# Performance work log

Hardware: AMD Instinct MI355X
Metric: run time of the kernel (lower is better)

The kernel has to match this reference:

```python
import jax, jax.numpy as jnp
import numpy as np

EPS = 1e-12  # torch F.normalize eps

def _l2norm(x):
    n = jnp.linalg.norm(x, axis=-1, keepdims=True)
    return x / jnp.maximum(n, EPS)

def _encode(h, mask, W, b):
    # h: [B,S,H], mask: [B,S] int
    h = h * mask[..., None].astype(h.dtype)      # zero padded tokens
    pooled = h[:, 0]                             # pooling_type='cls'
    col = h[:, 1:] @ W + b                       # colbert_linear on tokens 1:
    return _l2norm(pooled), _l2norm(col)         # normalize=True


def setup_inputs() -> dict:
    key = jax.random.key(0)
    k1, k2, k3, k4, k5, k6 = jax.random.split(key, 6)
    Q, Sq, C, Sc, H, D = 64, 32, 256, 256, 768, 128
    return {
        "q_hidden": jax.random.normal(k1, (Q, Sq, H), jnp.float32),
        "c_hidden": jax.random.normal(k2, (C, Sc, H), jnp.float32),
        "W": jax.random.normal(k3, (H, D), jnp.float32) / np.sqrt(H).astype(np.float32),
        "b": jax.random.normal(k4, (D,), jnp.float32) * 0.01,
        "q_mask": jax.random.randint(k5, (Q, Sq), 0, 2, jnp.int32),
        "c_mask": jax.random.randint(k6, (C, Sc), 0, 2, jnp.int32),
    }


def reference(q_hidden, c_hidden, W, b, q_mask, c_mask):
    q_pooled, q_col = _encode(q_hidden, q_mask, W, b)   # q_col: [Q, Sq-1, D]
    c_pooled, c_col = _encode(c_hidden, c_mask, W, b)   # c_col: [C, Sc-1, D]
    # MaxSim late interaction (get_batch_colbert_sim)
    token_sim = jnp.einsum('qin,cjn->qicj', q_col, c_col)  # [Q, Sq-1, C, Sc-1]
    sim = token_sim.max(axis=-1)                           # max over doc tokens j
    denom = q_mask[:, 1:].sum(-1, keepdims=True).astype(sim.dtype)
    sim = sim.sum(axis=1) / denom                          # [Q, C]
    return sim, q_pooled, c_pooled
```

## Files before the change

kernel.cpp:

```cpp
#include <hip/hip_runtime.h>
#include <hip/hip_bf16.h>

#define QN 64
#define SQ 32
#define CN 256
#define SC 256
#define HD 768
#define DD 128

typedef __attribute__((ext_vector_type(8))) short short8;
typedef __attribute__((ext_vector_type(4))) float f32x4;

static __device__ __forceinline__ unsigned short f2bf(float x) {
  unsigned u = __float_as_uint(x);
  unsigned r = 0x7FFFu + ((u >> 16) & 1u);
  return (unsigned short)((u + r) >> 16);
}
static __device__ __forceinline__ unsigned pack2(float a, float b) {
  return (unsigned)f2bf(a) | ((unsigned)f2bf(b) << 16);
}

typedef const __attribute__((address_space(1))) unsigned int* as1_u32p;
typedef __attribute__((address_space(3))) unsigned int* as3_u32p;
static __device__ __forceinline__ void gl_lds16(const void* g, void* l) {
  __builtin_amdgcn_global_load_lds((as1_u32p)g, (as3_u32p)l, 16, 0, 0);
}

__global__ __launch_bounds__(256) void prep_kernel(
    const float* __restrict__ W,
    const float* __restrict__ qh, const int* __restrict__ qm,
    const float* __restrict__ ch, const int* __restrict__ cm,
    unsigned short* __restrict__ WtS,
    float* __restrict__ outq, float* __restrict__ outc,
    unsigned short* __restrict__ qcolP) {
  __shared__ float red[4];
  int bid = blockIdx.x, tid = threadIdx.x;

  if (bid < DD) {
    int d = bid;
    if (tid < 96) {
      int kc = tid;
      unsigned p[4];
#pragma unroll
      for (int e = 0; e < 4; ++e) {
        float a = W[(size_t)(kc * 8 + 2 * e) * DD + d];
        float b = W[(size_t)(kc * 8 + 2 * e + 1) * DD + d];
        p[e] = pack2(a, b);
      }
      int kcp = (kc & ~7) | ((kc & 7) ^ (d & 7));
      *(uint4*)&WtS[((size_t)d * 96 + kcp) * 8] = *(uint4*)p;
    }
    return;
  }

  int row = bid - DD;
  const float* src;
  float* dst;
  float m;
  if (row < QN) {
    src = qh + (size_t)row * SQ * HD;
    m = (float)qm[row * SQ];
    dst = outq + (size_t)row * HD;
  } else {
    int b = row - QN;
    src = ch + (size_t)b * SC * HD;
    m = (float)cm[b * SC];
    dst = outc + (size_t)b * HD;
  }
  float ss = 0.f;
  for (int k = tid; k < HD; k += 256) {
    float v = src[k] * m;
    ss += v * v;
  }
  int lane = tid & 63, wv = tid >> 6;
  for (int off = 32; off; off >>= 1) ss += __shfl_xor(ss, off);
  if (lane == 0) red[wv] = ss;
  __syncthreads();
  float tot = red[0] + red[1] + red[2] + red[3];
  float inv = 1.f / fmaxf(sqrtf(tot), 1e-12f);
  for (int k = tid; k < HD; k += 256) dst[k] = src[k] * m * inv;
  if (row < QN && tid < 64)
    ((unsigned*)(qcolP + ((size_t)row * 32 + 31) * DD))[tid] = 0u;
}

union ProjLDS {
  unsigned short b[128 * 32 * 8];
  float cep[128 * 132];
};

__global__ __launch_bounds__(256, 2) void proj_kernel(
    const float* __restrict__ q_hidden, const float* __restrict__ c_hidden,
    const int* __restrict__ q_mask, const int* __restrict__ c_mask,
    const unsigned short* __restrict__ WtS, const float* __restrict__ bias,
    unsigned short* __restrict__ qcol, unsigned short* __restrict__ ccol) {
  __shared__ ProjLDS u;
  int bx = blockIdx.x;
  int isQ = (bx >= 510) ? 1 : 0;
  int base = isQ ? (bx - 510) : bx;
  int tid = threadIdx.x, lane = tid & 63, wv = tid >> 6;
  int lm = lane & 15, lq = lane >> 4;

  const float* hrow[2];
#pragma unroll
  for (int mt = 0; mt < 2; ++mt) {
    int g = base * 128 + wv * 32 + mt * 16 + lm;
    const float* hp;
    if (isQ) {
      g = (g < 1983) ? g : 1983;
      int qq = g / 31, t = g - qq * 31;
      hp = q_hidden + ((size_t)qq * SQ + t + 1) * HD;
    } else {
      int cb = g / 255, t = g - cb * 255;
      hp = c_hidden + ((size_t)cb * SC + t + 1) * HD;
    }
    hrow[mt] = hp;
  }

  f32x4 acc[2][8];
#pragma unroll
  for (int i = 0; i < 2; ++i)
#pragma unroll
    for (int j = 0; j < 8; ++j) acc[i][j] = (f32x4){0.f, 0.f, 0.f, 0.f};

  for (int stage = 0; stage < 3; ++stage) {
    __syncthreads();
#pragma unroll
    for (int i = 0; i < 16; ++i) {
      int d = i * 8 + wv * 2 + (lane >> 5);
      int lc = lane & 31;
      gl_lds16(WtS + ((size_t)d * 96 + stage * 32 + lc) * 8,
               (char*)u.b + (size_t)(i * 256 + wv * 64) * 16);
    }
    __syncthreads();

#pragma unroll
    for (int w = 0; w < 8; ++w) {
      int kwin = stage * 8 + w;
      short8 afr[2];
#pragma unroll
      for (int mt = 0; mt < 2; ++mt) {
        const float* ha = hrow[mt] + kwin * 32 + lq * 8;
        float4 a0 = *(const float4*)ha;
        float4 a1 = *(const float4*)(ha + 4);
        unsigned p[4];
        p[0] = pack2(a0.x, a0.y); p[1] = pack2(a0.z, a0.w);
        p[2] = pack2(a1.x, a1.y); p[3] = pack2(a1.z, a1.w);
        afr[mt] = *(short8*)p;
      }
      int t = w * 4 + lq;
      int lcp = (t & ~7) | ((t & 7) ^ (lm & 7));
      short8 bfr[8];
#pragma unroll
      for (int nt = 0; nt < 8; ++nt) {
        int ci = (nt * 16 + lm) * 32 + lcp;
        bfr[nt] = *(const short8*)&u.b[(size_t)ci * 8];
      }
#pragma unroll
      for (int mt = 0; mt < 2; ++mt)
#pragma unroll
        for (int nt = 0; nt < 8; ++nt)
          acc[mt][nt] = __builtin_amdgcn_mfma_f32_16x16x32_bf16(afr[mt], bfr[nt], acc[mt][nt], 0, 0, 0);
    }
  }

  __syncthreads();
#pragma unroll
  for (int mt = 0; mt < 2; ++mt)
#pragma unroll
    for (int nt = 0; nt < 8; ++nt)
#pragma unroll
      for (int r = 0; r < 4; ++r) {
        int rw = wv * 32 + mt * 16 + lq * 4 + r;
        int col = nt * 16 + lm;
        u.cep[rw * 132 + col] = acc[mt][nt][r];
      }
  __syncthreads();

  int tk = tid >> 1, hf = tid & 1;
  int g = base * 128 + tk;
  int qq, t, valid = 1;
  float fm;
  if (isQ) {
    if (g >= 1983) { valid = (g == 1983); g = 1983; }
    qq = g / 31; t = g - qq * 31;
    fm = (float)q_mask[qq * SQ + t + 1];
  } else {
    qq = g / 255; t = g - qq * 255;
    fm = (float)c_mask[qq * SC + t + 1];
  }

  float v[64];
  float ss = 0.f;
#pragma unroll
  for (int j = 0; j < 16; ++j) {
    float4 cv = *(const float4*)&u.cep[tk * 132 + hf * 64 + j * 4];
    float4 bv = *(const float4*)&bias[hf * 64 + j * 4];
    v[4 * j + 0] = cv.x * fm + bv.x; v[4 * j + 1] = cv.y * fm + bv.y;
    v[4 * j + 2] = cv.z * fm + bv.z; v[4 * j + 3] = cv.w * fm + bv.w;
#pragma unroll
    for (int e = 0; e < 4; ++e) ss += v[4 * j + e] * v[4 * j + e];
  }
  ss += __shfl_xor(ss, 1);
  float inv = 1.f / fmaxf(sqrtf(ss), 1e-12f);

  uint4 pk4[8];
#pragma unroll
  for (int j = 0; j < 8; ++j) {
    unsigned p[4];
#pragma unroll
    for (int e = 0; e < 4; ++e)
      p[e] = pack2(v[8 * j + 2 * e] * inv, v[8 * j + 2 * e + 1] * inv);
    pk4[j] = *(uint4*)p;
  }

  if (isQ) {
    if (valid) {
      uint4* dst = (uint4*)(qcol + ((size_t)qq * 32 + t) * DD + hf * 64);
#pragma unroll
      for (int j = 0; j < 8; ++j) dst[j] = pk4[j];
    }
  } else {
    uint4* rowp = (uint4*)(ccol + ((size_t)qq * 256 + t) * DD);
#pragma unroll
    for (int j = 0; j < 8; ++j) {
      int kc = hf * 8 + j;
      int p = (kc & 8) | ((kc & 7) ^ (t & 7));
      rowp[p] = pk4[j];
    }
    if (t == 254) {
      uint4* rowp2 = rowp + 8;
#pragma unroll
      for (int j = 0; j < 8; ++j) {
        int kc = hf * 8 + j;
        int p = (kc & 8) | ((kc & 7) ^ 7);
        rowp2[p] = pk4[j];
      }
    }
  }
}

__global__ __launch_bounds__(256, 2) void sim_kernel(
    const unsigned short* __restrict__ qcolP,
    const unsigned short* __restrict__ ccol,
    const int* __restrict__ qmask,
    float* __restrict__ sim) {
  __shared__ unsigned short cbuf[256 * 128];
  int tid = threadIdx.x, lane = tid & 63, wv = tid >> 6;
  int lm = lane & 15, lq = lane >> 4;
  int qb = blockIdx.y * 8 + wv * 2;
  int c0 = blockIdx.x * 4;

  short8 af[2][2][4];
#pragma unroll
  for (int q2 = 0; q2 < 2; ++q2)
#pragma unroll
    for (int it = 0; it < 2; ++it)
#pragma unroll
      for (int kf = 0; kf < 4; ++kf)
        af[q2][it][kf] = *(const short8*)(qcolP +
            (((size_t)(qb + q2) * 32 + it * 16 + lm) * DD + kf * 32 + lq * 8));

  float dinv[2];
#pragma unroll
  for (int q2 = 0; q2 < 2; ++q2) {
    float v = (lane >= 1 && lane < 32) ? (float)qmask[(qb + q2) * SQ + lane] : 0.f;
    for (int off = 1; off < 64; off <<= 1) v += __shfl_xor(v, off);
    dinv[q2] = 1.f / v;
  }

  for (int cc = 0; cc < 4; ++cc) {
    int c = c0 + cc;
    __syncthreads();
    const unsigned short* src = ccol + (size_t)c * SC * DD;
#pragma unroll
    for (int i = 0; i < 16; ++i) {
      gl_lds16(src + (size_t)(i * 256 + wv * 64 + lane) * 8,
               (char*)cbuf + (size_t)(i * 256 + wv * 64) * 16);
    }
    __syncthreads();

    float rmax[2][2];
#pragma unroll
    for (int q2 = 0; q2 < 2; ++q2) { rmax[q2][0] = -__builtin_inff(); rmax[q2][1] = -__builtin_inff(); }

    for (int jt = 0; jt < 16; ++jt) {
      short8 cf[4];
#pragma unroll
      for (int kf = 0; kf < 4; ++kf) {
        int row = jt * 16 + lm;
        int kc = kf * 4 + lq;
        int p = (kc & 8) | ((kc & 7) ^ (row & 7));
        cf[kf] = *(const short8*)&cbuf[(size_t)(row * 16 + p) * 8];
      }
#pragma unroll
      for (int q2 = 0; q2 < 2; ++q2)
#pragma unroll
        for (int it = 0; it < 2; ++it) {
          f32x4 acc = (f32x4){0.f, 0.f, 0.f, 0.f};
#pragma unroll
          for (int kf = 0; kf < 4; ++kf)
            acc = __builtin_amdgcn_mfma_f32_16x16x32_bf16(cf[kf], af[q2][it][kf], acc, 0, 0, 0);
          float loc = fmaxf(fmaxf(acc[0], acc[1]), fmaxf(acc[2], acc[3]));
          rmax[q2][it] = fmaxf(rmax[q2][it], loc);
        }
    }

#pragma unroll
    for (int q2 = 0; q2 < 2; ++q2) {
      float m0 = rmax[q2][0], m1 = rmax[q2][1];
      m0 = fmaxf(m0, __shfl_xor(m0, 16)); m0 = fmaxf(m0, __shfl_xor(m0, 32));
      m1 = fmaxf(m1, __shfl_xor(m1, 16)); m1 = fmaxf(m1, __shfl_xor(m1, 32));
      float s = m0 + ((lm == 15) ? 0.f : m1);
      s += __shfl_xor(s, 1); s += __shfl_xor(s, 2);
      s += __shfl_xor(s, 4); s += __shfl_xor(s, 8);
      if (lane == 0) sim[(qb + q2) * CN + c] = s * dinv[q2];
    }
  }
}

extern "C" void kernel_launch(void* const* d_in, const int* in_sizes, int n_in,
                              void* d_out, int out_size, void* d_ws, size_t ws_size,
                              hipStream_t stream) {
  const float* q_hidden = (const float*)d_in[0];
  const float* c_hidden = (const float*)d_in[1];
  const float* W = (const float*)d_in[2];
  const float* bias = (const float*)d_in[3];
  const int* q_mask = (const int*)d_in[4];
  const int* c_mask = (const int*)d_in[5];

  float* out = (float*)d_out;
  float* sim = out;
  float* q_pooled = out + QN * CN;
  float* c_pooled = q_pooled + QN * HD;

  unsigned short* WtS   = (unsigned short*)d_ws;
  unsigned short* qcolP = (unsigned short*)((char*)d_ws + (256 << 10));
  unsigned short* ccol  = (unsigned short*)((char*)d_ws + (1 << 20));

  prep_kernel<<<DD + QN + CN, 256, 0, stream>>>(W, q_hidden, q_mask, c_hidden, c_mask,
                                                WtS, q_pooled, c_pooled, qcolP);
  proj_kernel<<<526, 256, 0, stream>>>(q_hidden, c_hidden, q_mask, c_mask,
                                       WtS, bias, qcolP, ccol);
  sim_kernel<<<dim3(64, 8), 256, 0, stream>>>(qcolP, ccol, q_mask, sim);
}
```

Measured before the change: 374.7 us.

## Stage activations via LDS in projection and enlarge per-wave query tile in sim

The projection kernel now copies fp32 activation tiles and bf16 weight tiles into shared memory with async global-to-LDS loads over 12 k-steps, using swizzled indexing, instead of reading activations straight from global memory per wave. Its epilogue is split into two 64-row halves so the LDS union shrinks, and launch bounds rise to 3 blocks per CU to allow more occupancy. The sim kernel gives each wave 4 queries over 2 docs instead of 2 queries over 4 docs, which reuses each loaded doc tile across more queries. The cost is more barriers per k-loop in the projection kernel and higher register pressure in sim from the larger query fragment array.

Measured after the change: 363.7 us. 1.03x faster.

```diff
diff --git a/kernel.cpp b/kernel.cpp
--- a/kernel.cpp
+++ b/kernel.cpp
@@ -84,11 +84,11 @@
 }
 
 union ProjLDS {
-  unsigned short b[128 * 32 * 8];
-  float cep[128 * 132];
+  struct { float a[128 * 64]; unsigned short w[128 * 64]; } s;
+  float cep[64 * 132];
 };
 
-__global__ __launch_bounds__(256, 2) void proj_kernel(
+__global__ __launch_bounds__(256, 3) void proj_kernel(
     const float* __restrict__ q_hidden, const float* __restrict__ c_hidden,
     const int* __restrict__ q_mask, const int* __restrict__ c_mask,
     const unsigned short* __restrict__ WtS, const float* __restrict__ bias,
@@ -100,10 +100,12 @@
   int tid = threadIdx.x, lane = tid & 63, wv = tid >> 6;
   int lm = lane & 15, lq = lane >> 4;
 
-  const float* hrow[2];
-#pragma unroll
-  for (int mt = 0; mt < 2; ++mt) {
-    int g = base * 128 + wv * 32 + mt * 16 + lm;
+  int ac = (tid & 8) | ((tid & 7) ^ ((tid >> 4) & 7));
+  const float* aptr[8];
+#pragma unroll
+  for (int i = 0; i < 8; ++i) {
+    int r = i * 16 + (tid >> 4);
+    int g = base * 128 + r;
     const float* hp;
     if (isQ) {
       g = (g < 1983) ? g : 1983;
@@ -113,7 +115,13 @@
       int cb = g / 255, t = g - cb * 255;
       hp = c_hidden + ((size_t)cb * SC + t + 1) * HD;
     }
-    hrow[mt] = hp;
+    aptr[i] = hp + ac * 4;
+  }
+  const unsigned short* wptr[4];
+#pragma unroll
+  for (int i = 0; i < 4; ++i) {
+    int d = i * 32 + (tid >> 3);
+    wptr[i] = WtS + ((size_t)d * 96 + (tid & 7)) * 8;
   }
 
   f32x4 acc[2][8];
@@ -122,38 +130,37 @@
 #pragma unroll
     for (int j = 0; j < 8; ++j) acc[i][j] = (f32x4){0.f, 0.f, 0.f, 0.f};
 
-  for (int stage = 0; stage < 3; ++stage) {
-    __syncthreads();
-#pragma unroll
-    for (int i = 0; i < 16; ++i) {
-      int d = i * 8 + wv * 2 + (lane >> 5);
-      int lc = lane & 31;
-      gl_lds16(WtS + ((size_t)d * 96 + stage * 32 + lc) * 8,
-               (char*)u.b + (size_t)(i * 256 + wv * 64) * 16);
-    }
-    __syncthreads();
-
-#pragma unroll
-    for (int w = 0; w < 8; ++w) {
-      int kwin = stage * 8 + w;
+  for (int step = 0; step < 12; ++step) {
+    __syncthreads();
+#pragma unroll
+    for (int i = 0; i < 8; ++i)
+      gl_lds16(aptr[i] + step * 64, (char*)u.s.a + (size_t)(i * 256 + wv * 64) * 16);
+#pragma unroll
+    for (int i = 0; i < 4; ++i)
+      gl_lds16(wptr[i] + step * 64, (char*)u.s.w + (size_t)(i * 256 + wv * 64) * 16);
+    __syncthreads();
+
+#pragma unroll
+    for (int w = 0; w < 2; ++w) {
       short8 afr[2];
 #pragma unroll
       for (int mt = 0; mt < 2; ++mt) {
-        const float* ha = hrow[mt] + kwin * 32 + lq * 8;
-        float4 a0 = *(const float4*)ha;
-        float4 a1 = *(const float4*)(ha + 4);
+        int rr = wv * 32 + mt * 16 + lm;
+        int x0 = (lq * 2) ^ (lm & 7);
+        int x1 = (lq * 2 + 1) ^ (lm & 7);
+        float4 a0 = *(const float4*)&u.s.a[rr * 64 + w * 32 + x0 * 4];
+        float4 a1 = *(const float4*)&u.s.a[rr * 64 + w * 32 + x1 * 4];
         unsigned p[4];
         p[0] = pack2(a0.x, a0.y); p[1] = pack2(a0.z, a0.w);
         p[2] = pack2(a1.x, a1.y); p[3] = pack2(a1.z, a1.w);
         afr[mt] = *(short8*)p;
       }
-      int t = w * 4 + lq;
-      int lcp = (t & ~7) | ((t & 7) ^ (lm & 7));
       short8 bfr[8];
 #pragma unroll
       for (int nt = 0; nt < 8; ++nt) {
-        int ci = (nt * 16 + lm) * 32 + lcp;
-        bfr[nt] = *(const short8*)&u.b[(size_t)ci * 8];
+        int d = nt * 16 + lm;
+        int pc = (w * 4 + lq) ^ (lm & 7);
+        bfr[nt] = *(const short8*)&u.s.w[d * 64 + pc * 8];
       }
 #pragma unroll
       for (int mt = 0; mt < 2; ++mt)
@@ -163,77 +170,82 @@
     }
   }
 
-  __syncthreads();
-#pragma unroll
-  for (int mt = 0; mt < 2; ++mt)
-#pragma unroll
-    for (int nt = 0; nt < 8; ++nt)
-#pragma unroll
-      for (int r = 0; r < 4; ++r) {
-        int rw = wv * 32 + mt * 16 + lq * 4 + r;
-        int col = nt * 16 + lm;
-        u.cep[rw * 132 + col] = acc[mt][nt][r];
-      }
-  __syncthreads();
-
-  int tk = tid >> 1, hf = tid & 1;
-  int g = base * 128 + tk;
-  int qq, t, valid = 1;
-  float fm;
-  if (isQ) {
-    if (g >= 1983) { valid = (g == 1983); g = 1983; }
-    qq = g / 31; t = g - qq * 31;
-    fm = (float)q_mask[qq * SQ + t + 1];
-  } else {
-    qq = g / 255; t = g - qq * 255;
-    fm = (float)c_mask[qq * SC + t + 1];
-  }
-
-  float v[64];
-  float ss = 0.f;
-#pragma unroll
-  for (int j = 0; j < 16; ++j) {
-    float4 cv = *(const float4*)&u.cep[tk * 132 + hf * 64 + j * 4];
-    float4 bv = *(const float4*)&bias[hf * 64 + j * 4];
-    v[4 * j + 0] = cv.x * fm + bv.x; v[4 * j + 1] = cv.y * fm + bv.y;
-    v[4 * j + 2] = cv.z * fm + bv.z; v[4 * j + 3] = cv.w * fm + bv.w;
-#pragma unroll
-    for (int e = 0; e < 4; ++e) ss += v[4 * j + e] * v[4 * j + e];
-  }
-  ss += __shfl_xor(ss, 1);
-  float inv = 1.f / fmaxf(sqrtf(ss), 1e-12f);
-
-  uint4 pk4[8];
-#pragma unroll
-  for (int j = 0; j < 8; ++j) {
-    unsigned p[4];
-#pragma unroll
-    for (int e = 0; e < 4; ++e)
-      p[e] = pack2(v[8 * j + 2 * e] * inv, v[8 * j + 2 * e + 1] * inv);
-    pk4[j] = *(uint4*)p;
-  }
-
-  if (isQ) {
-    if (valid) {
-      uint4* dst = (uint4*)(qcol + ((size_t)qq * 32 + t) * DD + hf * 64);
-#pragma unroll
-      for (int j = 0; j < 8; ++j) dst[j] = pk4[j];
-    }
-  } else {
-    uint4* rowp = (uint4*)(ccol + ((size_t)qq * 256 + t) * DD);
+  int tk = tid >> 2, qt = tid & 3;
+#pragma unroll
+  for (int h = 0; h < 2; ++h) {
+    __syncthreads();
+    if ((wv >> 1) == h) {
+#pragma unroll
+      for (int mt = 0; mt < 2; ++mt)
+#pragma unroll
+        for (int nt = 0; nt < 8; ++nt)
+#pragma unroll
+          for (int r = 0; r < 4; ++r) {
+            int row = (wv & 1) * 32 + mt * 16 + lq * 4 + r;
+            u.cep[row * 132 + nt * 16 + lm] = acc[mt][nt][r];
+          }
+    }
+    __syncthreads();
+
+    int g = base * 128 + h * 64 + tk;
+    int qq, t, valid = 1;
+    float fm;
+    if (isQ) {
+      if (g > 1983) { valid = 0; g = 1983; }
+      qq = g / 31; t = g - qq * 31;
+      fm = (float)q_mask[qq * SQ + t + 1];
+    } else {
+      qq = g / 255; t = g - qq * 255;
+      fm = (float)c_mask[qq * SC + t + 1];
+    }
+
+    float v[32];
+    float ss = 0.f;
 #pragma unroll
     for (int j = 0; j < 8; ++j) {
-      int kc = hf * 8 + j;
-      int p = (kc & 8) | ((kc & 7) ^ (t & 7));
-      rowp[p] = pk4[j];
-    }
-    if (t == 254) {
-      uint4* rowp2 = rowp + 8;
-#pragma unroll
-      for (int j = 0; j < 8; ++j) {
-        int kc = hf * 8 + j;
-        int p = (kc & 8) | ((kc & 7) ^ 7);
-        rowp2[p] = pk4[j];
+      float4 cv = *(const float4*)&u.cep[tk * 132 + qt * 32 + j * 4];
+      float4 bv = *(const float4*)&bias[qt * 32 + j * 4];
+      v[4 * j + 0] = cv.x * fm + bv.x; v[4 * j + 1] = cv.y * fm + bv.y;
+      v[4 * j + 2] = cv.z * fm + bv.z; v[4 * j + 3] = cv.w * fm + bv.w;
+#pragma unroll
+      for (int e = 0; e < 4; ++e) ss += v[4 * j + e] * v[4 * j + e];
+    }
+    ss += __shfl_xor(ss, 1);
+    ss += __shfl_xor(ss, 2);
+    float inv = 1.f / fmaxf(sqrtf(ss), 1e-12f);
+
+    uint4 pk4[4];
+#pragma unroll
+    for (int j = 0; j < 4; ++j) {
+      unsigned p[4];
+#pragma unroll
+      for (int e = 0; e < 4; ++e)
+        p[e] = pack2(v[8 * j + 2 * e] * inv, v[8 * j + 2 * e + 1] * inv);
+      pk4[j] = *(uint4*)p;
+    }
+
+    if (isQ) {
+      if (valid) {
+        uint4* dst = (uint4*)(qcol + ((size_t)qq * 32 + t) * DD + qt * 32);
+#pragma unroll
+        for (int j = 0; j < 4; ++j) dst[j] = pk4[j];
+      }
+    } else {
+      uint4* rowp = (uint4*)(ccol + ((size_t)qq * 256 + t) * DD);
+#pragma unroll
+      for (int j = 0; j < 4; ++j) {
+        int kc = qt * 4 + j;
+        int p = (kc & 8) | ((kc & 7) ^ (t & 7));
+        rowp[p] = pk4[j];
+      }
+      if (t == 254) {
+        uint4* rowp2 = rowp + 8;
+#pragma unroll
+        for (int j = 0; j < 4; ++j) {
+          int kc = qt * 4 + j;
+          int p = (kc & 8) | ((kc & 7) ^ 7);
+          rowp2[p] = pk4[j];
+        }
       }
     }
   }
@@ -247,12 +259,12 @@
   __shared__ unsigned short cbuf[256 * 128];
   int tid = threadIdx.x, lane = tid & 63, wv = tid >> 6;
   int lm = lane & 15, lq = lane >> 4;
-  int qb = blockIdx.y * 8 + wv * 2;
-  int c0 = blockIdx.x * 4;
-
-  short8 af[2][2][4];
-#pragma unroll
-  for (int q2 = 0; q2 < 2; ++q2)
+  int qb = blockIdx.y * 16 + wv * 4;
+  int c0 = blockIdx.x * 2;
+
+  short8 af[4][2][4];
+#pragma unroll
+  for (int q2 = 0; q2 < 4; ++q2)
 #pragma unroll
     for (int it = 0; it < 2; ++it)
 #pragma unroll
@@ -260,28 +272,27 @@
         af[q2][it][kf] = *(const short8*)(qcolP +
             (((size_t)(qb + q2) * 32 + it * 16 + lm) * DD + kf * 32 + lq * 8));
 
-  float dinv[2];
-#pragma unroll
-  for (int q2 = 0; q2 < 2; ++q2) {
+  float dinv[4];
+#pragma unroll
+  for (int q2 = 0; q2 < 4; ++q2) {
     float v = (lane >= 1 && lane < 32) ? (float)qmask[(qb + q2) * SQ + lane] : 0.f;
     for (int off = 1; off < 64; off <<= 1) v += __shfl_xor(v, off);
     dinv[q2] = 1.f / v;
   }
 
-  for (int cc = 0; cc < 4; ++cc) {
+  for (int cc = 0; cc < 2; ++cc) {
     int c = c0 + cc;
     __syncthreads();
     const unsigned short* src = ccol + (size_t)c * SC * DD;
 #pragma unroll
-    for (int i = 0; i < 16; ++i) {
+    for (int i = 0; i < 16; ++i)
       gl_lds16(src + (size_t)(i * 256 + wv * 64 + lane) * 8,
                (char*)cbuf + (size_t)(i * 256 + wv * 64) * 16);
-    }
-    __syncthreads();
-
-    float rmax[2][2];
-#pragma unroll
-    for (int q2 = 0; q2 < 2; ++q2) { rmax[q2][0] = -__builtin_inff(); rmax[q2][1] = -__builtin_inff(); }
+    __syncthreads();
+
+    float rmax[4][2];
+#pragma unroll
+    for (int q2 = 0; q2 < 4; ++q2) { rmax[q2][0] = -__builtin_inff(); rmax[q2][1] = -__builtin_inff(); }
 
     for (int jt = 0; jt < 16; ++jt) {
       short8 cf[4];
@@ -293,7 +304,7 @@
         cf[kf] = *(const short8*)&cbuf[(size_t)(row * 16 + p) * 8];
       }
 #pragma unroll
-      for (int q2 = 0; q2 < 2; ++q2)
+      for (int q2 = 0; q2 < 4; ++q2)
 #pragma unroll
         for (int it = 0; it < 2; ++it) {
           f32x4 acc = (f32x4){0.f, 0.f, 0.f, 0.f};
@@ -306,7 +317,7 @@
     }
 
 #pragma unroll
-    for (int q2 = 0; q2 < 2; ++q2) {
+    for (int q2 = 0; q2 < 4; ++q2) {
       float m0 = rmax[q2][0], m1 = rmax[q2][1];
       m0 = fmaxf(m0, __shfl_xor(m0, 16)); m0 = fmaxf(m0, __shfl_xor(m0, 32));
       m1 = fmaxf(m1, __shfl_xor(m1, 16)); m1 = fmaxf(m1, __shfl_xor(m1, 32));
@@ -341,5 +352,5 @@
                                                 WtS, q_pooled, c_pooled, qcolP);
   proj_kernel<<<526, 256, 0, stream>>>(q_hidden, c_hidden, q_mask, c_mask,
                                        WtS, bias, qcolP, ccol);
-  sim_kernel<<<dim3(64, 8), 256, 0, stream>>>(qcolP, ccol, q_mask, sim);
-}
+  sim_kernel<<<dim3(128, 4), 256, 0, stream>>>(qcolP, ccol, q_mask, sim);
+}
```

## Split projection into single-wave blocks with register-prefetched weights and retile MaxSim

Applied to the files above, without the earlier changes.

The projection kernel drops the LDS-staged swizzled weight tile. Each 64-thread block now handles 32 tokens and streams a plain [D,H] bf16 weight layout straight into registers, with one-step software prefetch of activations and weights. The similarity kernel now gives each wave 4 queries and each block 2 documents, so every document tile loaded into LDS is reused across more queries. The duplicate padding-row write also changes its offset from 8 to 16 uint4, which lands it on the next row. The cost is more global/L2 weight traffic per block and higher register pressure in both kernels.

New measurement: 369.1 us. About the same (-1.5%).

```diff
diff --git a/kernel.cpp b/kernel.cpp
--- a/kernel.cpp
+++ b/kernel.cpp
@@ -38,18 +38,8 @@
 
   if (bid < DD) {
     int d = bid;
-    if (tid < 96) {
-      int kc = tid;
-      unsigned p[4];
-#pragma unroll
-      for (int e = 0; e < 4; ++e) {
-        float a = W[(size_t)(kc * 8 + 2 * e) * DD + d];
-        float b = W[(size_t)(kc * 8 + 2 * e + 1) * DD + d];
-        p[e] = pack2(a, b);
-      }
-      int kcp = (kc & ~7) | ((kc & 7) ^ (d & 7));
-      *(uint4*)&WtS[((size_t)d * 96 + kcp) * 8] = *(uint4*)p;
-    }
+    for (int k = tid; k < HD; k += 256)
+      WtS[(size_t)d * HD + k] = f2bf(W[(size_t)k * DD + d]);
     return;
   }
 
@@ -83,38 +73,31 @@
     ((unsigned*)(qcolP + ((size_t)row * 32 + 31) * DD))[tid] = 0u;
 }
 
-union ProjLDS {
-  unsigned short b[128 * 32 * 8];
-  float cep[128 * 132];
-};
-
-__global__ __launch_bounds__(256, 2) void proj_kernel(
+__global__ __launch_bounds__(64, 2) void proj_kernel(
     const float* __restrict__ q_hidden, const float* __restrict__ c_hidden,
     const int* __restrict__ q_mask, const int* __restrict__ c_mask,
     const unsigned short* __restrict__ WtS, const float* __restrict__ bias,
     unsigned short* __restrict__ qcol, unsigned short* __restrict__ ccol) {
-  __shared__ ProjLDS u;
+  __shared__ float cep[32 * 132];
   int bx = blockIdx.x;
-  int isQ = (bx >= 510) ? 1 : 0;
-  int base = isQ ? (bx - 510) : bx;
-  int tid = threadIdx.x, lane = tid & 63, wv = tid >> 6;
+  int isQ = (bx >= 2040) ? 1 : 0;
+  int tokbase = (isQ ? (bx - 2040) : bx) * 32;
+  int lane = threadIdx.x & 63;
   int lm = lane & 15, lq = lane >> 4;
 
-  const float* hrow[2];
+  const float* arow[2];
 #pragma unroll
   for (int mt = 0; mt < 2; ++mt) {
-    int g = base * 128 + wv * 32 + mt * 16 + lm;
-    const float* hp;
+    int g = tokbase + mt * 16 + lm;
     if (isQ) {
-      g = (g < 1983) ? g : 1983;
       int qq = g / 31, t = g - qq * 31;
-      hp = q_hidden + ((size_t)qq * SQ + t + 1) * HD;
+      arow[mt] = q_hidden + ((size_t)qq * SQ + t + 1) * HD + lq * 8;
     } else {
       int cb = g / 255, t = g - cb * 255;
-      hp = c_hidden + ((size_t)cb * SC + t + 1) * HD;
-    }
-    hrow[mt] = hp;
-  }
+      arow[mt] = c_hidden + ((size_t)cb * SC + t + 1) * HD + lq * 8;
+    }
+  }
+  const unsigned short* wrow = WtS + (size_t)lm * HD + lq * 8;
 
   f32x4 acc[2][8];
 #pragma unroll
@@ -122,66 +105,70 @@
 #pragma unroll
     for (int j = 0; j < 8; ++j) acc[i][j] = (f32x4){0.f, 0.f, 0.f, 0.f};
 
-  for (int stage = 0; stage < 3; ++stage) {
-    __syncthreads();
-#pragma unroll
-    for (int i = 0; i < 16; ++i) {
-      int d = i * 8 + wv * 2 + (lane >> 5);
-      int lc = lane & 31;
-      gl_lds16(WtS + ((size_t)d * 96 + stage * 32 + lc) * 8,
-               (char*)u.b + (size_t)(i * 256 + wv * 64) * 16);
-    }
-    __syncthreads();
-
-#pragma unroll
-    for (int w = 0; w < 8; ++w) {
-      int kwin = stage * 8 + w;
-      short8 afr[2];
+  float4 pa[2][2];
+  short8 pw[8];
+#pragma unroll
+  for (int mt = 0; mt < 2; ++mt) {
+    pa[mt][0] = *(const float4*)(arow[mt]);
+    pa[mt][1] = *(const float4*)(arow[mt] + 4);
+  }
+#pragma unroll
+  for (int nt = 0; nt < 8; ++nt)
+    pw[nt] = *(const short8*)(wrow + (size_t)nt * 16 * HD);
+
+  for (int w = 0; w < 24; ++w) {
+    float4 ca[2][2];
+    short8 cw[8];
+#pragma unroll
+    for (int mt = 0; mt < 2; ++mt) { ca[mt][0] = pa[mt][0]; ca[mt][1] = pa[mt][1]; }
+#pragma unroll
+    for (int nt = 0; nt < 8; ++nt) cw[nt] = pw[nt];
+
+    if (w < 23) {
+      int ko = (w + 1) * 32;
 #pragma unroll
       for (int mt = 0; mt < 2; ++mt) {
-        const float* ha = hrow[mt] + kwin * 32 + lq * 8;
-        float4 a0 = *(const float4*)ha;
-        float4 a1 = *(const float4*)(ha + 4);
-        unsigned p[4];
-        p[0] = pack2(a0.x, a0.y); p[1] = pack2(a0.z, a0.w);
-        p[2] = pack2(a1.x, a1.y); p[3] = pack2(a1.z, a1.w);
-        afr[mt] = *(short8*)p;
+        pa[mt][0] = *(const float4*)(arow[mt] + ko);
+        pa[mt][1] = *(const float4*)(arow[mt] + ko + 4);
       }
-      int t = w * 4 + lq;
-      int lcp = (t & ~7) | ((t & 7) ^ (lm & 7));
-      short8 bfr[8];
-#pragma unroll
-      for (int nt = 0; nt < 8; ++nt) {
-        int ci = (nt * 16 + lm) * 32 + lcp;
-        bfr[nt] = *(const short8*)&u.b[(size_t)ci * 8];
-      }
-#pragma unroll
-      for (int mt = 0; mt < 2; ++mt)
-#pragma unroll
-        for (int nt = 0; nt < 8; ++nt)
-          acc[mt][nt] = __builtin_amdgcn_mfma_f32_16x16x32_bf16(afr[mt], bfr[nt], acc[mt][nt], 0, 0, 0);
-    }
-  }
-
-  __syncthreads();
+#pragma unroll
+      for (int nt = 0; nt < 8; ++nt)
+        pw[nt] = *(const short8*)(wrow + (size_t)nt * 16 * HD + ko);
+    }
+
+    short8 afr[2];
+#pragma unroll
+    for (int mt = 0; mt < 2; ++mt) {
+      unsigned p[4];
+      p[0] = pack2(ca[mt][0].x, ca[mt][0].y);
+      p[1] = pack2(ca[mt][0].z, ca[mt][0].w);
+      p[2] = pack2(ca[mt][1].x, ca[mt][1].y);
+      p[3] = pack2(ca[mt][1].z, ca[mt][1].w);
+      afr[mt] = *(short8*)p;
+    }
+#pragma unroll
+    for (int mt = 0; mt < 2; ++mt)
+#pragma unroll
+      for (int nt = 0; nt < 8; ++nt)
+        acc[mt][nt] = __builtin_amdgcn_mfma_f32_16x16x32_bf16(afr[mt], cw[nt], acc[mt][nt], 0, 0, 0);
+  }
+
 #pragma unroll
   for (int mt = 0; mt < 2; ++mt)
 #pragma unroll
     for (int nt = 0; nt < 8; ++nt)
 #pragma unroll
       for (int r = 0; r < 4; ++r) {
-        int rw = wv * 32 + mt * 16 + lq * 4 + r;
-        int col = nt * 16 + lm;
-        u.cep[rw * 132 + col] = acc[mt][nt][r];
+        int row = mt * 16 + lq * 4 + r;
+        cep[row * 132 + nt * 16 + lm] = acc[mt][nt][r];
       }
   __syncthreads();
 
-  int tk = tid >> 1, hf = tid & 1;
-  int g = base * 128 + tk;
-  int qq, t, valid = 1;
+  int r2 = lane >> 1, hf = lane & 1;
+  int g = tokbase + r2;
+  int qq, t;
   float fm;
   if (isQ) {
-    if (g >= 1983) { valid = (g == 1983); g = 1983; }
     qq = g / 31; t = g - qq * 31;
     fm = (float)q_mask[qq * SQ + t + 1];
   } else {
@@ -193,7 +180,7 @@
   float ss = 0.f;
 #pragma unroll
   for (int j = 0; j < 16; ++j) {
-    float4 cv = *(const float4*)&u.cep[tk * 132 + hf * 64 + j * 4];
+    float4 cv = *(const float4*)&cep[r2 * 132 + hf * 64 + j * 4];
     float4 bv = *(const float4*)&bias[hf * 64 + j * 4];
     v[4 * j + 0] = cv.x * fm + bv.x; v[4 * j + 1] = cv.y * fm + bv.y;
     v[4 * j + 2] = cv.z * fm + bv.z; v[4 * j + 3] = cv.w * fm + bv.w;
@@ -214,11 +201,9 @@
   }
 
   if (isQ) {
-    if (valid) {
-      uint4* dst = (uint4*)(qcol + ((size_t)qq * 32 + t) * DD + hf * 64);
-#pragma unroll
-      for (int j = 0; j < 8; ++j) dst[j] = pk4[j];
-    }
+    uint4* dst = (uint4*)(qcol + ((size_t)qq * 32 + t) * DD) + hf * 8;
+#pragma unroll
+    for (int j = 0; j < 8; ++j) dst[j] = pk4[j];
   } else {
     uint4* rowp = (uint4*)(ccol + ((size_t)qq * 256 + t) * DD);
 #pragma unroll
@@ -228,7 +213,7 @@
       rowp[p] = pk4[j];
     }
     if (t == 254) {
-      uint4* rowp2 = rowp + 8;
+      uint4* rowp2 = rowp + 16;
 #pragma unroll
       for (int j = 0; j < 8; ++j) {
         int kc = hf * 8 + j;
@@ -247,12 +232,12 @@
   __shared__ unsigned short cbuf[256 * 128];
   int tid = threadIdx.x, lane = tid & 63, wv = tid >> 6;
   int lm = lane & 15, lq = lane >> 4;
-  int qb = blockIdx.y * 8 + wv * 2;
-  int c0 = blockIdx.x * 4;
-
-  short8 af[2][2][4];
-#pragma unroll
-  for (int q2 = 0; q2 < 2; ++q2)
+  int qb = blockIdx.y * 16 + wv * 4;
+  int c0 = blockIdx.x * 2;
+
+  short8 af[4][2][4];
+#pragma unroll
+  for (int q2 = 0; q2 < 4; ++q2)
 #pragma unroll
     for (int it = 0; it < 2; ++it)
 #pragma unroll
@@ -260,28 +245,27 @@
         af[q2][it][kf] = *(const short8*)(qcolP +
             (((size_t)(qb + q2) * 32 + it * 16 + lm) * DD + kf * 32 + lq * 8));
 
-  float dinv[2];
-#pragma unroll
-  for (int q2 = 0; q2 < 2; ++q2) {
+  float dinv[4];
+#pragma unroll
+  for (int q2 = 0; q2 < 4; ++q2) {
     float v = (lane >= 1 && lane < 32) ? (float)qmask[(qb + q2) * SQ + lane] : 0.f;
     for (int off = 1; off < 64; off <<= 1) v += __shfl_xor(v, off);
     dinv[q2] = 1.f / v;
   }
 
-  for (int cc = 0; cc < 4; ++cc) {
+  for (int cc = 0; cc < 2; ++cc) {
     int c = c0 + cc;
     __syncthreads();
     const unsigned short* src = ccol + (size_t)c * SC * DD;
 #pragma unroll
-    for (int i = 0; i < 16; ++i) {
+    for (int i = 0; i < 16; ++i)
       gl_lds16(src + (size_t)(i * 256 + wv * 64 + lane) * 8,
                (char*)cbuf + (size_t)(i * 256 + wv * 64) * 16);
-    }
     __syncthreads();
 
-    float rmax[2][2];
-#pragma unroll
-    for (int q2 = 0; q2 < 2; ++q2) { rmax[q2][0] = -__builtin_inff(); rmax[q2][1] = -__builtin_inff(); }
+    float rmax[4][2];
+#pragma unroll
+    for (int q2 = 0; q2 < 4; ++q2) { rmax[q2][0] = -__builtin_inff(); rmax[q2][1] = -__builtin_inff(); }
 
     for (int jt = 0; jt < 16; ++jt) {
       short8 cf[4];
@@ -293,7 +277,7 @@
         cf[kf] = *(const short8*)&cbuf[(size_t)(row * 16 + p) * 8];
       }
 #pragma unroll
-      for (int q2 = 0; q2 < 2; ++q2)
+      for (int q2 = 0; q2 < 4; ++q2)
 #pragma unroll
         for (int it = 0; it < 2; ++it) {
           f32x4 acc = (f32x4){0.f, 0.f, 0.f, 0.f};
@@ -306,7 +290,7 @@
     }
 
 #pragma unroll
-    for (int q2 = 0; q2 < 2; ++q2) {
+    for (int q2 = 0; q2 < 4; ++q2) {
       float m0 = rmax[q2][0], m1 = rmax[q2][1];
       m0 = fmaxf(m0, __shfl_xor(m0, 16)); m0 = fmaxf(m0, __shfl_xor(m0, 32));
       m1 = fmaxf(m1, __shfl_xor(m1, 16)); m1 = fmaxf(m1, __shfl_xor(m1, 32));
@@ -339,7 +323,7 @@
 
   prep_kernel<<<DD + QN + CN, 256, 0, stream>>>(W, q_hidden, q_mask, c_hidden, c_mask,
                                                 WtS, q_pooled, c_pooled, qcolP);
-  proj_kernel<<<526, 256, 0, stream>>>(q_hidden, c_hidden, q_mask, c_mask,
+  proj_kernel<<<2102, 64, 0, stream>>>(q_hidden, c_hidden, q_mask, c_mask,
                                        WtS, bias, qcolP, ccol);
-  sim_kernel<<<dim3(64, 8), 256, 0, stream>>>(qcolP, ccol, q_mask, sim);
-}
+  sim_kernel<<<dim3(128, 4), 256, 0, stream>>>(qcolP, ccol, q_mask, sim);
+}
```
